# Kernel tuning notes

Measured on AMD Instinct MI355X. Metric: run time of the kernel, lower is better.

## Reference

```python
import jax, jax.numpy as jnp
import numpy as np

B, R, T = 128, 36, 40
E, V, H1, H2, PH, VOC = 1024, 2048, 1024, 1024, 256, 10000


def _lstm_cell(x, h, c, Wi, Wh, b):
    # torch gate order: i, f, g, o
    g = x @ Wi.T + h @ Wh.T + b
    i, f, gg, o = jnp.split(g, 4, axis=-1)
    c_new = jax.nn.sigmoid(f) * c + jax.nn.sigmoid(i) * jnp.tanh(gg)
    h_new = jax.nn.sigmoid(o) * jnp.tanh(c_new)
    return h_new, c_new


def setup_inputs() -> dict:
    key = jax.random.key(0)
    ks = jax.random.split(key, 20)
    s = 0.05
    Vmat = jax.random.normal(ks[0], (B, R, V), jnp.float32)
    enc_features = jax.random.normal(ks[1], (B, V), jnp.float32)
    union_vfeats = jax.random.normal(ks[2], (B, V), jnp.float32)
    captions = jax.random.randint(ks[3], (B, T), 0, VOC, jnp.int32)
    lengths = jax.random.randint(ks[4], (B,), 1, T + 1, jnp.int32)
    lengths = jnp.sort(lengths)[::-1].at[0].set(T)  # sorted descending, max first
    embed_W = jax.random.normal(ks[5], (VOC, E), jnp.float32) * s
    Wi1 = jax.random.normal(ks[6], (4 * H1, H2 + V + E), jnp.float32) * s
    Wh1 = jax.random.normal(ks[7], (4 * H1, H1), jnp.float32) * s
    b1 = jax.random.normal(ks[8], (4 * H1,), jnp.float32) * s
    Wi2 = jax.random.normal(ks[9], (4 * H2, H1 + V), jnp.float32) * s
    Wh2 = jax.random.normal(ks[10], (4 * H2, H2), jnp.float32) * s
    b2 = jax.random.normal(ks[11], (4 * H2,), jnp.float32) * s
    Wva = jax.random.normal(ks[12], (PH, V), jnp.float32) * s
    bva = jax.random.normal(ks[13], (PH,), jnp.float32) * s
    Wha = jax.random.normal(ks[14], (PH, H1), jnp.float32) * s
    bha = jax.random.normal(ks[15], (PH,), jnp.float32) * s
    wa = jax.random.normal(ks[16], (PH,), jnp.float32) * s
    ba = jax.random.normal(ks[17], (), jnp.float32) * s
    Wl = jax.random.normal(ks[18], (VOC, H2), jnp.float32) * s
    bl = jax.random.normal(ks[19], (VOC,), jnp.float32) * s
    return dict(Vmat=Vmat, enc_features=enc_features, union_vfeats=union_vfeats,
                captions=captions, lengths=lengths, embed_W=embed_W,
                Wi1=Wi1, Wh1=Wh1, b1=b1, Wi2=Wi2, Wh2=Wh2, b2=b2,
                Wva=Wva, bva=bva, Wha=Wha, bha=bha, wa=wa, ba=ba, Wl=Wl, bl=bl)


def reference(Vmat, enc_features, union_vfeats, captions, lengths, embed_W,
              Wi1, Wh1, b1, Wi2, Wh2, b2, Wva, bva, Wha, bha, wa, ba, Wl, bl):
    embeddings = embed_W[captions]                      # [B, T, E]
    Va = Vmat @ Wva.T + bva                             # [B, R, PH] (precompute, step-invariant)

    def step(carry, xs):
        h1, c1, h2, c2 = carry
        emb_t, i = xs
        active = (lengths > i)[:, None]                 # [B, 1]
        x1 = jnp.concatenate([h2, union_vfeats, emb_t], axis=-1)
        h1n, c1n = _lstm_cell(x1, h1, c1, Wi1, Wh1, b1)
        # top-down attention over R regions
        logit = jnp.tanh(Va + (h1n @ Wha.T + bha)[:, None, :]) @ wa + ba  # [B, R]
        atten = jax.nn.softmax(logit, axis=1)
        av = jnp.einsum('br,brd->bd', atten, Vmat)      # [B, V]
        x2 = jnp.concatenate([av, h1n], axis=-1)
        h2n, c2n = _lstm_cell(x2, h2, c2, Wi2, Wh2, b2)
        logits = h2n @ Wl.T + bl                        # [B, VOC]
        # state freeze + zero outputs for finished sequences (ragged masking)
        h1 = jnp.where(active, h1n, h1); c1 = jnp.where(active, c1n, c1)
        h2 = jnp.where(active, h2n, h2); c2 = jnp.where(active, c2n, c2)
        out_t = jnp.where(active, logits, 0.0)
        return (h1, c1, h2, c2), out_t

    z1 = jnp.zeros((B, H1), jnp.float32)
    z2 = jnp.zeros((B, H2), jnp.float32)
    xs = (jnp.transpose(embeddings, (1, 0, 2)), jnp.arange(T, dtype=jnp.int32))
    _, outs = jax.lax.scan(step, (z1, z1, z2, z2), xs)  # [T, B, VOC]
    return jnp.transpose(outs, (1, 0, 2))               # [B, T, VOC]
```

## Files before the change

kernel.cpp:

```cpp
#include <hip/hip_runtime.h>

#define EPI_PART 0
#define EPI_BF16D 1

#define T_ 40
#define VOC_ 10000

typedef __attribute__((ext_vector_type(8))) short bf16x8;
typedef __attribute__((ext_vector_type(4))) short short4v;
typedef __attribute__((ext_vector_type(8))) short short8v;
typedef __attribute__((ext_vector_type(4))) float float4v;
typedef __attribute__((ext_vector_type(4))) float f32x4;

__device__ __forceinline__ float bf2f(short s) {
  unsigned u = ((unsigned)(unsigned short)s) << 16;
  float f; __builtin_memcpy(&f, &u, 4); return f;
}
__device__ __forceinline__ short f2bf(float f) {
  unsigned u; __builtin_memcpy(&u, &f, 4);
  u += 0x7FFFu + ((u >> 16) & 1u);
  return (short)(u >> 16);
}
__device__ __forceinline__ float sigm(float x) { return 1.f / (1.f + expf(-x)); }

__device__ __forceinline__ size_t pkidx(int row, int k, int K) {
  return (size_t)(row >> 4) * 16 * K + (size_t)(k >> 3) * 128 + (size_t)((row & 15) * 8 + (k & 7));
}


__global__ __launch_bounds__(256) void k_f2bf_split(const float* __restrict__ s,
    short* __restrict__ dh, short* __restrict__ dl, long n4) {
  long i = (long)blockIdx.x * 256 + threadIdx.x;
  long stride = (long)gridDim.x * 256;
  for (; i < n4; i += stride) {
    float4v f = ((const float4v*)s)[i];
    short4v oh, ol;
    #pragma unroll
    for (int j = 0; j < 4; j++) {
      short h = f2bf(f[j]); oh[j] = h; ol[j] = f2bf(f[j] - bf2f(h));
    }
    ((short4v*)dh)[i] = oh;
    ((short4v*)dl)[i] = ol;
  }
}

__global__ __launch_bounds__(256) void k_permpk(short* __restrict__ dh, short* __restrict__ dl,
    const float* __restrict__ s1, int ld1, int col0, int K1,
    const float* __restrict__ s2, int ld2, int Ktot) {
  int K4 = Ktot >> 2;
  long n4 = 4096L * K4;
  long stride = (long)gridDim.x * 256;
  for (long i = (long)blockIdx.x * 256 + threadIdx.x; i < n4; i += stride) {
    int p = (int)(i / K4);
    int c = ((int)(i % K4)) << 2;
    int orig = ((p & 3) << 10) + (p >> 2);
    const float* src = (c < K1) ? (s1 + (long)orig * ld1 + col0 + c)
                                : (s2 + (long)orig * ld2 + (c - K1));
    float4v f = *(const float4v*)src;
    short4v oh, ol;
    #pragma unroll
    for (int j = 0; j < 4; j++) {
      short h = f2bf(f[j]); oh[j] = h; ol[j] = f2bf(f[j] - bf2f(h));
    }
    size_t d = pkidx(p, c, Ktot);
    *(short4v*)&dh[d] = oh;
    if (dl) *(short4v*)&dl[d] = ol;
  }
}

__global__ __launch_bounds__(256) void k_packpk(short* __restrict__ dh, short* __restrict__ dl,
    const float* __restrict__ src, int ld, int Nr, int Nsrc, int K) {
  int K4 = K >> 2;
  long n4 = (long)Nr * K4;
  long stride = (long)gridDim.x * 256;
  for (long i = (long)blockIdx.x * 256 + threadIdx.x; i < n4; i += stride) {
    int row = (int)(i / K4);
    int c = ((int)(i % K4)) << 2;
    float4v f = {0.f, 0.f, 0.f, 0.f};
    if (row < Nsrc) f = *(const float4v*)(src + (long)row * ld + c);
    short4v oh, ol;
    #pragma unroll
    for (int j = 0; j < 4; j++) {
      short h = f2bf(f[j]); oh[j] = h; ol[j] = f2bf(f[j] - bf2f(h));
    }
    size_t d = pkidx(row, c, K);
    *(short4v*)&dh[d] = oh;
    if (dl) *(short4v*)&dl[d] = ol;
  }
}

__global__ __launch_bounds__(256) void k_perm_bias(float* __restrict__ d1, const float* __restrict__ s1,
                                                   float* __restrict__ d2, const float* __restrict__ s2) {
  int p = blockIdx.x * 256 + threadIdx.x;
  if (p < 4096) {
    int orig = ((p & 3) << 10) + (p >> 2);
    d1[p] = s1[orig];
    d2[p] = s2[orig];
  }
}

__global__ __launch_bounds__(256) void k_gather_emb(short* __restrict__ dst, const float* __restrict__ embW,
                                                    const int* __restrict__ cap) {
  int i = blockIdx.x * 256 + threadIdx.x;
  if (i >= 5120 * 128) return;
  int row = i >> 7, c8 = (i & 127) << 3;
  int tok = cap[row];
  const float4v* s = (const float4v*)(embW + (long)tok * 1024 + c8);
  float4v f0 = s[0], f1 = s[1];
  short8v o;
  #pragma unroll
  for (int j = 0; j < 4; j++) { o[j] = f2bf(f0[j]); o[4 + j] = f2bf(f1[j]); }
  *(short8v*)(dst + (long)row * 1024 + c8) = o;
}


template<int NC, bool SA, bool SW, int EPI>
__global__ __launch_bounds__(256) void k_g3(
    const short* __restrict__ A, const short* __restrict__ Alo, int lda,
    const short* __restrict__ W, const short* __restrict__ Wlo, int K,
    int Npad, int Mtot,
    float* __restrict__ outf, short* __restrict__ outbf) {
  __shared__ short sh[SA ? 32768 : 16384];
  const int tid = threadIdx.x;
  const int l = tid & 63, w = tid >> 6;
  const int rif = l & 15, kg = l >> 4;
  const int n0 = blockIdx.x * 64;
  const int k0 = blockIdx.y * NC * 128;
  const int mbase = blockIdx.z * 128;

  f32x4 acc[8];
  #pragma unroll
  for (int m = 0; m < 8; m++) acc[m] = (f32x4){0.f, 0.f, 0.f, 0.f};

  bf16x8 wh[2][4], wl[2][4];
  const size_t wtile = (size_t)(n0 / 16 + w) * 16 * K + (size_t)l * 8;

  auto loadW = [&](int c, int slot) {
    size_t base = wtile + (size_t)((k0 + c * 128) >> 3) * 128;
    #pragma unroll
    for (int sk = 0; sk < 4; sk++) {
      wh[slot][sk] = *(const bf16x8*)(W + base + sk * 512);
      if (SW) wl[slot][sk] = *(const bf16x8*)(Wlo + base + sk * 512);
    }
  };
  auto stageA = [&](int c) {
    #pragma unroll
    for (int p = 0; p < (SA ? 2 : 1); p++) {
      const short* src = p ? Alo : A;
      #pragma unroll
      for (int j = 0; j < 8; j++) {
        int row = (j * 4 + w) * 4 + (l >> 4);
        int col = (l & 15) * 8;
        short8v v = *(const short8v*)(src + (size_t)(mbase + row) * lda + k0 + c * 128 + col);
        *(short8v*)&sh[p * 16384 + row * 128 + (col ^ ((row & 7) << 3))] = v;
      }
    }
  };
  auto compute = [&](int slot) {
    #pragma unroll
    for (int sk = 0; sk < 4; sk++) {
      int colb = ((sk * 32 + kg * 8) ^ ((rif & 7) << 3));
      #pragma unroll
      for (int m = 0; m < 8; m++) {
        int idx = (m * 16 + rif) * 128 + colb;
        bf16x8 ah = *(const bf16x8*)&sh[idx];
        acc[m] = __builtin_amdgcn_mfma_f32_16x16x32_bf16(ah, wh[slot][sk], acc[m], 0, 0, 0);
        if (SA) {
          bf16x8 al = *(const bf16x8*)&sh[16384 + idx];
          acc[m] = __builtin_amdgcn_mfma_f32_16x16x32_bf16(al, wh[slot][sk], acc[m], 0, 0, 0);
        }
        if (SW) acc[m] = __builtin_amdgcn_mfma_f32_16x16x32_bf16(ah, wl[slot][sk], acc[m], 0, 0, 0);
      }
    }
  };

  loadW(0, 0);
  stageA(0);
  __syncthreads();
  #pragma unroll
  for (int c = 0; c < NC; c++) {
    if (c + 1 < NC) loadW(c + 1, (c + 1) & 1);
    compute(c & 1);
    if (c + 1 < NC) {
      __syncthreads();
      stageA(c + 1);
      __syncthreads();
    }
  }

  const int col = n0 + w * 16 + rif;
  #pragma unroll
  for (int m = 0; m < 8; m++) {
    #pragma unroll
    for (int j = 0; j < 4; j++) {
      int row = m * 16 + kg * 4 + j;
      if constexpr (EPI == EPI_PART) {
        outf[((size_t)blockIdx.y * Mtot + mbase + row) * Npad + col] = acc[m][j];
      } else {
        outbf[(size_t)(mbase + row) * Npad + col] = f2bf(acc[m][j]);
      }
    }
  }
}

__global__ __launch_bounds__(256) void k_sum(const float* __restrict__ part,
    float* __restrict__ out, const float* __restrict__ bias,
    long n4, int N4, int KS, long stride4) {
  long i = (long)blockIdx.x * 256 + threadIdx.x;
  if (i >= n4) return;
  float4v a = *(const float4v*)&bias[(i % N4) * 4];
  for (int s = 0; s < KS; s++) {
    float4v p = ((const float4v*)part)[s * stride4 + i];
    #pragma unroll
    for (int j = 0; j < 4; j++) a[j] += p[j];
  }
  ((float4v*)out)[i] = a;
}

template<int L, int KS>
__global__ __launch_bounds__(256) void k_epi(
    const float* __restrict__ part,
    const float* __restrict__ zuv, const short* __restrict__ zemb, const float* __restrict__ b2p,
    float* __restrict__ cstate,
    const short* __restrict__ xcur_hi, const short* __restrict__ xcur_lo,
    short* __restrict__ xnext_hi, short* __restrict__ xnext_lo,
    short* __restrict__ x2_hi, short* __restrict__ x2_lo,
    short* __restrict__ h2n_hi, short* __restrict__ h2n_lo,
    const int* __restrict__ lengths, int t) {
  int i = blockIdx.x * 256 + threadIdx.x;
  int b = i >> 10, h = i & 1023;
  float4v g = {0.f, 0.f, 0.f, 0.f};
  #pragma unroll
  for (int s = 0; s < KS; s++) {
    float4v p = *(const float4v*)&part[((size_t)s * 128 + b) * 4096 + h * 4];
    #pragma unroll
    for (int j = 0; j < 4; j++) g[j] += p[j];
  }
  if constexpr (L == 1) {
    float4v z = *(const float4v*)&zuv[(size_t)b * 4096 + h * 4];
    short4v e = *(const short4v*)&zemb[((size_t)b * T_ + t) * 4096 + h * 4];
    #pragma unroll
    for (int j = 0; j < 4; j++) g[j] += z[j] + bf2f(e[j]);
  } else {
    float4v z = *(const float4v*)&b2p[h * 4];
    #pragma unroll
    for (int j = 0; j < 4; j++) g[j] += z[j];
  }
  float co = cstate[b * 1024 + h];
  float cn = sigm(g[1]) * co + sigm(g[0]) * tanhf(g[2]);
  float hn = sigm(g[3]) * tanhf(cn);
  bool act = lengths[b] > t;
  cstate[b * 1024 + h] = act ? cn : co;
  short hi16 = f2bf(hn);
  short lo16 = f2bf(hn - bf2f(hi16));
  if constexpr (L == 1) {
    x2_hi[b * 4096 + 2048 + h] = hi16;
    x2_lo[b * 4096 + 2048 + h] = lo16;
    short oh = xcur_hi[b * 2048 + 1024 + h];
    short ol = xcur_lo[b * 2048 + 1024 + h];
    xnext_hi[b * 2048 + 1024 + h] = act ? hi16 : oh;
    xnext_lo[b * 2048 + 1024 + h] = act ? lo16 : ol;
    x2_hi[b * 4096 + 3072 + h] = xcur_hi[b * 2048 + h];
    x2_lo[b * 4096 + 3072 + h] = xcur_lo[b * 2048 + h];
  } else {
    h2n_hi[b * 1024 + h] = hi16;
    h2n_lo[b * 1024 + h] = lo16;
    short oh = xcur_hi[b * 2048 + h];
    short ol = xcur_lo[b * 2048 + h];
    xnext_hi[b * 2048 + h] = act ? hi16 : oh;
    xnext_lo[b * 2048 + h] = act ? lo16 : ol;
  }
}

__global__ __launch_bounds__(256) void k_epi_logits(const float* __restrict__ part,
    const float* __restrict__ bl, const int* __restrict__ lengths, int t,
    float* __restrict__ out) {
  int id = blockIdx.x * 256 + threadIdx.x;
  if (id >= 320000) return;
  int b = id / 2500, q = (id % 2500) * 4;
  bool act = lengths[b] > t;
  float4v a = {0.f, 0.f, 0.f, 0.f};
  if (act) {
    a = *(const float4v*)&bl[q];
    #pragma unroll
    for (int s = 0; s < 4; s++) {
      float4v p = *(const float4v*)&part[((size_t)s * 128 + b) * 10048 + q];
      #pragma unroll
      for (int j = 0; j < 4; j++) a[j] += p[j];
    }
  }
  *(float4v*)&out[((size_t)b * T_ + t) * VOC_ + q] = a;
}

__global__ __launch_bounds__(256) void k_attn(
    short* __restrict__ x2_hi, short* __restrict__ x2_lo,
    const float* __restrict__ haPart, const float* __restrict__ bha,
    const float* __restrict__ wa, const float* __restrict__ ba,
    const float* __restrict__ Va, const float* __restrict__ Vmat) {
  const int b = blockIdx.x, tid = threadIdx.x;
  __shared__ float ha_sh[256];
  __shared__ float wa_sh[256];
  __shared__ float logit_sh[40];
  __shared__ float p_sh[40];
  {
    float ha = bha[tid];
    #pragma unroll
    for (int s = 0; s < 8; s++) ha += haPart[((size_t)s * 128 + b) * 256 + tid];
    ha_sh[tid] = ha;
    wa_sh[tid] = wa[tid];
  }
  __syncthreads();
  {
    const int r0 = tid >> 3, sl = tid & 7;
    const float ba0 = ba[0];
    for (int r = r0; r < 36; r += 32) {
      const float4v* va4 = (const float4v*)(Va + ((long)b * 36 + r) * 256 + sl * 32);
      float part = 0.f;
      #pragma unroll
      for (int q = 0; q < 8; q++) {
        float4v v4 = va4[q];
        #pragma unroll
        for (int j = 0; j < 4; j++) {
          int ph = sl * 32 + q * 4 + j;
          part += tanhf(v4[j] + ha_sh[ph]) * wa_sh[ph];
        }
      }
      part += __shfl_down(part, 4, 8);
      part += __shfl_down(part, 2, 8);
      part += __shfl_down(part, 1, 8);
      if (sl == 0) logit_sh[r] = part + ba0;
    }
  }
  __syncthreads();
  if (tid < 64) {
    float v = (tid < 36) ? logit_sh[tid] : -3.4e38f;
    float m = v;
    #pragma unroll
    for (int off = 32; off > 0; off >>= 1) m = fmaxf(m, __shfl_xor(m, off));
    float e = (tid < 36) ? expf(v - m) : 0.f;
    float s = e;
    #pragma unroll
    for (int off = 32; off > 0; off >>= 1) s += __shfl_xor(s, off);
    if (tid < 36) p_sh[tid] = e / s;
  }
  __syncthreads();
  {
    float av[8];
    #pragma unroll
    for (int j = 0; j < 8; j++) av[j] = 0.f;
    const float* vb = Vmat + (long)b * (36 * 2048) + tid * 8;
    for (int r = 0; r < 36; r++) {
      float p = p_sh[r];
      float4v v0 = *(const float4v*)(vb + (long)r * 2048);
      float4v v1 = *(const float4v*)(vb + (long)r * 2048 + 4);
      #pragma unroll
      for (int j = 0; j < 4; j++) { av[j] += p * v0[j]; av[4 + j] += p * v1[j]; }
    }
    short8v oh, ol;
    #pragma unroll
    for (int j = 0; j < 8; j++) {
      short h = f2bf(av[j]);
      oh[j] = h;
      ol[j] = f2bf(av[j] - bf2f(h));
    }
    *(short8v*)(x2_hi + b * 4096 + tid * 8) = oh;
    *(short8v*)(x2_lo + b * 4096 + tid * 8) = ol;
  }
}

extern "C" void kernel_launch(void* const* d_in, const int* in_sizes, int n_in,
                              void* d_out, int out_size, void* d_ws, size_t ws_size,
                              hipStream_t stream) {
  const float* Vmat = (const float*)d_in[0];
  const float* uv   = (const float*)d_in[2];
  const int* captions = (const int*)d_in[3];
  const int* lengths  = (const int*)d_in[4];
  const float* embW = (const float*)d_in[5];
  const float* Wi1 = (const float*)d_in[6];
  const float* Wh1 = (const float*)d_in[7];
  const float* b1  = (const float*)d_in[8];
  const float* Wi2 = (const float*)d_in[9];
  const float* Wh2 = (const float*)d_in[10];
  const float* b2  = (const float*)d_in[11];
  const float* Wva = (const float*)d_in[12];
  const float* bva = (const float*)d_in[13];
  const float* Wha = (const float*)d_in[14];
  const float* bha = (const float*)d_in[15];
  const float* wa  = (const float*)d_in[16];
  const float* ba  = (const float*)d_in[17];
  const float* Wl  = (const float*)d_in[18];
  const float* bl  = (const float*)d_in[19];
  (void)in_sizes; (void)n_in; (void)out_size; (void)ws_size;

  char* ws = (char*)d_ws;
  size_t off = 0;
  auto alloc = [&](size_t bytes) { void* p = ws + off; off += (bytes + 255) & ~255UL; return p; };
  short* W1dHi = (short*)alloc(4096L * 2048 * 2);
  short* W1dLo = (short*)alloc(4096L * 2048 * 2);
  short* W2dHi = (short*)alloc(4096L * 4096 * 2);
  short* W2dLo = (short*)alloc(4096L * 4096 * 2);
  short* WlPK  = (short*)alloc(10048L * 1024 * 2);
  short* WhaHi = (short*)alloc(256L * 1024 * 2);
  short* WhaLo = (short*)alloc(256L * 1024 * 2);
  float* VaBuf = (float*)alloc(4608L * 256 * 4);
  float* Z1uvB = (float*)alloc(128L * 4096 * 4);
  short* Z1embB = (short*)alloc(5120L * 4096 * 2);
  float* partG = (float*)alloc(16L * 128 * 4096 * 4);
  float* haPart = (float*)alloc(8L * 128 * 256 * 4);
  float* b1P = (float*)alloc(4096 * 4);
  float* b2P = (float*)alloc(4096 * 4);
  short* x1Hi = (short*)alloc(2L * 128 * 2048 * 2);
  short* x1Lo = (short*)alloc(2L * 128 * 2048 * 2);
  short* x2Hi = (short*)alloc(128L * 4096 * 2);
  short* x2Lo = (short*)alloc(128L * 4096 * 2);
  short* h2nHi = (short*)alloc(128L * 1024 * 2);
  short* h2nLo = (short*)alloc(128L * 1024 * 2);
  float* c1 = (float*)alloc(128L * 1024 * 4);
  float* c2 = (float*)alloc(128L * 1024 * 4);

  short* W1uvHi = W2dHi;
  short* W1uvLo = W2dHi + 4096L * 2048;
  float* zuvPart = (float*)(W2dHi + 4096L * 4096);
  short* uvHi = W2dHi + 4096L * 4096 + 4096L * 2048 + 2097152;
  short* uvLo = uvHi + 128L * 2048;
  short* WvaHi = uvLo + 128L * 2048;
  short* WvaLo = WvaHi + 256L * 2048;
  float* vaPart = (float*)W2dHi;
  short* W1ePk = (short*)partG;
  short* AembBF = (short*)partG + 4096L * 1024;
  short* VmatHi = Z1embB;
  short* VmatLo = Z1embB + 4608L * 2048;

  hipMemsetAsync(x1Hi, 0, 2L * 128 * 2048 * 2, stream);
  hipMemsetAsync(x1Lo, 0, 2L * 128 * 2048 * 2, stream);
  hipMemsetAsync(c1, 0, 128L * 1024 * 4, stream);
  hipMemsetAsync(c2, 0, 128L * 1024 * 4, stream);

  k_packpk<<<2048, 256, 0, stream>>>(WlPK, nullptr, Wl, 1024, 10048, 10000, 1024);
  k_packpk<<<256, 256, 0, stream>>>(WhaHi, WhaLo, Wha, 1024, 256, 256, 1024);
  k_packpk<<<512, 256, 0, stream>>>(WvaHi, WvaLo, Wva, 2048, 256, 256, 2048);
  k_permpk<<<2048, 256, 0, stream>>>(W1dHi, W1dLo, Wi1, 4096, 0, 1024, Wh1, 1024, 2048);
  k_permpk<<<2048, 256, 0, stream>>>(W1uvHi, W1uvLo, Wi1, 4096, 1024, 2048, Wi1, 4096, 2048);
  k_permpk<<<1024, 256, 0, stream>>>(W1ePk, nullptr, Wi1, 4096, 3072, 1024, Wi1, 4096, 1024);
  k_perm_bias<<<16, 256, 0, stream>>>(b1P, b1, b2P, b2);
  k_gather_emb<<<2560, 256, 0, stream>>>(AembBF, embW, captions);
  k_f2bf_split<<<2048, 256, 0, stream>>>(Vmat, VmatHi, VmatLo, 128L * 36 * 2048 / 4);
  k_f2bf_split<<<64, 256, 0, stream>>>(uv, uvHi, uvLo, 128L * 2048 / 4);

  k_g3<2, true, true, EPI_PART><<<dim3(64, 8, 1), 256, 0, stream>>>(
      uvHi, uvLo, 2048, W1uvHi, W1uvLo, 2048, 4096, 128, zuvPart, nullptr);
  k_sum<<<512, 256, 0, stream>>>(zuvPart, Z1uvB, b1P, 131072, 1024, 8, 131072);
  k_g3<2, true, true, EPI_PART><<<dim3(4, 8, 36), 256, 0, stream>>>(
      VmatHi, VmatLo, 2048, WvaHi, WvaLo, 2048, 256, 4608, vaPart, nullptr);
  k_sum<<<1152, 256, 0, stream>>>(vaPart, VaBuf, bva, 294912, 64, 8, 294912);
  k_permpk<<<4096, 256, 0, stream>>>(W2dHi, W2dLo, Wi2, 3072, 0, 3072, Wh2, 1024, 4096);
  k_g3<8, false, false, EPI_BF16D><<<dim3(64, 1, 40), 256, 0, stream>>>(
      AembBF, nullptr, 1024, W1ePk, nullptr, 1024, 4096, 5120, nullptr, Z1embB);

  for (int t = 0; t < T_; t++) {
    const short* xcH = x1Hi + (size_t)(t & 1) * (128 * 2048);
    const short* xcL = x1Lo + (size_t)(t & 1) * (128 * 2048);
    short* xnH = x1Hi + (size_t)((t + 1) & 1) * (128 * 2048);
    short* xnL = x1Lo + (size_t)((t + 1) & 1) * (128 * 2048);
    k_g3<2, true, true, EPI_PART><<<dim3(64, 8, 1), 256, 0, stream>>>(
        xcH, xcL, 2048, W1dHi, W1dLo, 2048, 4096, 128, partG, nullptr);
    k_epi<1, 8><<<512, 256, 0, stream>>>(partG, Z1uvB, Z1embB, nullptr, c1,
        xcH, xcL, xnH, xnL, x2Hi, x2Lo, nullptr, nullptr, lengths, t);
    k_g3<1, true, true, EPI_PART><<<dim3(4, 8, 1), 256, 0, stream>>>(
        x2Hi + 2048, x2Lo + 2048, 4096, WhaHi, WhaLo, 1024, 256, 128, haPart, nullptr);
    k_attn<<<128, 256, 0, stream>>>(x2Hi, x2Lo, haPart, bha, wa, ba, VaBuf, Vmat);
    k_g3<2, true, true, EPI_PART><<<dim3(64, 16, 1), 256, 0, stream>>>(
        x2Hi, x2Lo, 4096, W2dHi, W2dLo, 4096, 4096, 128, partG, nullptr);
    k_epi<2, 16><<<512, 256, 0, stream>>>(partG, nullptr, nullptr, b2P, c2,
        xcH, xcL, xnH, xnL, nullptr, nullptr, h2nHi, h2nLo, lengths, t);
    k_g3<2, true, false, EPI_PART><<<dim3(157, 4, 1), 256, 0, stream>>>(
        h2nHi, h2nLo, 1024, WlPK, nullptr, 1024, 10048, 128, partG, nullptr);
    k_epi_logits<<<1250, 256, 0, stream>>>(partG, bl, lengths, t, (float*)d_out);
  }
}
```

Measured before the change: 4.075 ms.

## Fuse split-K reductions and LSTM/logit epilogues into GEMM via last-block counters

Each split-K GEMM now writes its partials, then bumps an atomic per-tile counter. The last-arriving block reduces all K-slices and runs the epilogue in place: bias sum, LSTM cell update, or masked logits. This removes the separate k_sum, k_epi and k_epi_logits launches and their extra global passes. The second LSTM GEMM also changes split from 16 to 8 with NC 4, which halves the partial traffic but lengthens each block's K loop. The cost is threadfences and atomics, plus a serialized tail in which a single block per tile does the whole epilogue.

New measurement: 8.194 ms. +101.1%, slower.

```diff
diff --git a/kernel.cpp b/kernel.cpp
--- a/kernel.cpp
+++ b/kernel.cpp
@@ -1,7 +1,10 @@
 #include <hip/hip_runtime.h>
 
-#define EPI_PART 0
-#define EPI_BF16D 1
+#define EPI_BF16D 0
+#define EPI_SUMF32 1
+#define EPI_LSTM1 2
+#define EPI_LSTM2 3
+#define EPI_LOGITS 4
 
 #define T_ 40
 #define VOC_ 10000
@@ -114,12 +117,22 @@
 }
 
 
-template<int NC, bool SA, bool SW, int EPI>
-__global__ __launch_bounds__(256) void k_g3(
+template<int NC, int KS, bool SA, bool SW, int EPI>
+__global__ __launch_bounds__(256) void k_g4(
     const short* __restrict__ A, const short* __restrict__ Alo, int lda,
     const short* __restrict__ W, const short* __restrict__ Wlo, int K,
     int Npad, int Mtot,
-    float* __restrict__ outf, short* __restrict__ outbf) {
+    float* __restrict__ part, short* __restrict__ outbf,
+    int* __restrict__ cnt, int cbase,
+    const float* __restrict__ bias, float* __restrict__ outf, int outN,
+    const float* __restrict__ zuv, const short* __restrict__ zemb,
+    float* __restrict__ cstate,
+    const short* __restrict__ xcur_hi, const short* __restrict__ xcur_lo,
+    short* __restrict__ xnext_hi, short* __restrict__ xnext_lo,
+    short* __restrict__ x2_hi, short* __restrict__ x2_lo,
+    short* __restrict__ h2n_hi, short* __restrict__ h2n_lo,
+    const int* __restrict__ lengths, int t,
+    float* __restrict__ out_logits) {
   __shared__ short sh[SA ? 32768 : 16384];
   const int tid = threadIdx.x;
   const int l = tid & 63, w = tid >> 6;
@@ -188,127 +201,129 @@
     }
   }
 
-  const int col = n0 + w * 16 + rif;
+  const int colw = n0 + w * 16 + rif;
+  if constexpr (EPI == EPI_BF16D) {
+    #pragma unroll
+    for (int m = 0; m < 8; m++)
+      #pragma unroll
+      for (int j = 0; j < 4; j++)
+        outbf[(size_t)(mbase + m * 16 + kg * 4 + j) * Npad + colw] = f2bf(acc[m][j]);
+    return;
+  }
+
   #pragma unroll
-  for (int m = 0; m < 8; m++) {
-    #pragma unroll
-    for (int j = 0; j < 4; j++) {
-      int row = m * 16 + kg * 4 + j;
-      if constexpr (EPI == EPI_PART) {
-        outf[((size_t)blockIdx.y * Mtot + mbase + row) * Npad + col] = acc[m][j];
+  for (int m = 0; m < 8; m++)
+    #pragma unroll
+    for (int j = 0; j < 4; j++)
+      part[((size_t)blockIdx.y * Mtot + mbase + m * 16 + kg * 4 + j) * Npad + colw] = acc[m][j];
+
+  __shared__ int lastFlag;
+  __syncthreads();
+  if (tid == 0) {
+    __threadfence();
+    int old = atomicAdd(&cnt[cbase + blockIdx.x + gridDim.x * blockIdx.z], 1);
+    lastFlag = (old == KS - 1);
+  }
+  __syncthreads();
+  if (!lastFlag) return;
+  __threadfence();
+
+  if constexpr (EPI == EPI_SUMF32) {
+    for (int e = tid * 4; e < 8192; e += 1024) {
+      int row = e >> 6, c = e & 63;
+      int col = n0 + c;
+      float4v a = *(const float4v*)&bias[col];
+      #pragma unroll
+      for (int s = 0; s < KS; s++) {
+        float4v p = *(const float4v*)&part[((size_t)s * Mtot + mbase + row) * Npad + col];
+        #pragma unroll
+        for (int j = 0; j < 4; j++) a[j] += p[j];
+      }
+      *(float4v*)&outf[(size_t)(mbase + row) * outN + col] = a;
+    }
+  } else if constexpr (EPI == EPI_LOGITS) {
+    for (int e = tid * 4; e < 8192; e += 1024) {
+      int b = e >> 6, c = e & 63;
+      int col = n0 + c;
+      if (col < VOC_) {
+        bool act = lengths[b] > t;
+        float4v a = {0.f, 0.f, 0.f, 0.f};
+        if (act) {
+          a = *(const float4v*)&bias[col];
+          #pragma unroll
+          for (int s = 0; s < KS; s++) {
+            float4v p = *(const float4v*)&part[((size_t)s * 128 + b) * Npad + col];
+            #pragma unroll
+            for (int j = 0; j < 4; j++) a[j] += p[j];
+          }
+        }
+        *(float4v*)&out_logits[((size_t)b * T_ + t) * VOC_ + col] = a;
+      }
+    }
+  } else {
+    #pragma unroll
+    for (int i = 0; i < 8; i++) {
+      int pid = i * 256 + tid;
+      int b = pid >> 4, hl = pid & 15;
+      float4v g = {0.f, 0.f, 0.f, 0.f};
+      #pragma unroll
+      for (int s = 0; s < KS; s++) {
+        float4v p = *(const float4v*)&part[((size_t)s * 128 + b) * Npad + n0 + hl * 4];
+        #pragma unroll
+        for (int j = 0; j < 4; j++) g[j] += p[j];
+      }
+      if constexpr (EPI == EPI_LSTM1) {
+        float4v z = *(const float4v*)&zuv[(size_t)b * 4096 + n0 + hl * 4];
+        short4v e4 = *(const short4v*)&zemb[((size_t)b * T_ + t) * 4096 + n0 + hl * 4];
+        #pragma unroll
+        for (int j = 0; j < 4; j++) g[j] += z[j] + bf2f(e4[j]);
       } else {
-        outbf[(size_t)(mbase + row) * Npad + col] = f2bf(acc[m][j]);
-      }
-    }
-  }
-}
-
-__global__ __launch_bounds__(256) void k_sum(const float* __restrict__ part,
-    float* __restrict__ out, const float* __restrict__ bias,
-    long n4, int N4, int KS, long stride4) {
-  long i = (long)blockIdx.x * 256 + threadIdx.x;
-  if (i >= n4) return;
-  float4v a = *(const float4v*)&bias[(i % N4) * 4];
-  for (int s = 0; s < KS; s++) {
-    float4v p = ((const float4v*)part)[s * stride4 + i];
-    #pragma unroll
-    for (int j = 0; j < 4; j++) a[j] += p[j];
-  }
-  ((float4v*)out)[i] = a;
-}
-
-template<int L, int KS>
-__global__ __launch_bounds__(256) void k_epi(
-    const float* __restrict__ part,
-    const float* __restrict__ zuv, const short* __restrict__ zemb, const float* __restrict__ b2p,
-    float* __restrict__ cstate,
-    const short* __restrict__ xcur_hi, const short* __restrict__ xcur_lo,
-    short* __restrict__ xnext_hi, short* __restrict__ xnext_lo,
-    short* __restrict__ x2_hi, short* __restrict__ x2_lo,
-    short* __restrict__ h2n_hi, short* __restrict__ h2n_lo,
-    const int* __restrict__ lengths, int t) {
-  int i = blockIdx.x * 256 + threadIdx.x;
-  int b = i >> 10, h = i & 1023;
-  float4v g = {0.f, 0.f, 0.f, 0.f};
-  #pragma unroll
-  for (int s = 0; s < KS; s++) {
-    float4v p = *(const float4v*)&part[((size_t)s * 128 + b) * 4096 + h * 4];
-    #pragma unroll
-    for (int j = 0; j < 4; j++) g[j] += p[j];
-  }
-  if constexpr (L == 1) {
-    float4v z = *(const float4v*)&zuv[(size_t)b * 4096 + h * 4];
-    short4v e = *(const short4v*)&zemb[((size_t)b * T_ + t) * 4096 + h * 4];
-    #pragma unroll
-    for (int j = 0; j < 4; j++) g[j] += z[j] + bf2f(e[j]);
-  } else {
-    float4v z = *(const float4v*)&b2p[h * 4];
-    #pragma unroll
-    for (int j = 0; j < 4; j++) g[j] += z[j];
-  }
-  float co = cstate[b * 1024 + h];
-  float cn = sigm(g[1]) * co + sigm(g[0]) * tanhf(g[2]);
-  float hn = sigm(g[3]) * tanhf(cn);
-  bool act = lengths[b] > t;
-  cstate[b * 1024 + h] = act ? cn : co;
-  short hi16 = f2bf(hn);
-  short lo16 = f2bf(hn - bf2f(hi16));
-  if constexpr (L == 1) {
-    x2_hi[b * 4096 + 2048 + h] = hi16;
-    x2_lo[b * 4096 + 2048 + h] = lo16;
-    short oh = xcur_hi[b * 2048 + 1024 + h];
-    short ol = xcur_lo[b * 2048 + 1024 + h];
-    xnext_hi[b * 2048 + 1024 + h] = act ? hi16 : oh;
-    xnext_lo[b * 2048 + 1024 + h] = act ? lo16 : ol;
-    x2_hi[b * 4096 + 3072 + h] = xcur_hi[b * 2048 + h];
-    x2_lo[b * 4096 + 3072 + h] = xcur_lo[b * 2048 + h];
-  } else {
-    h2n_hi[b * 1024 + h] = hi16;
-    h2n_lo[b * 1024 + h] = lo16;
-    short oh = xcur_hi[b * 2048 + h];
-    short ol = xcur_lo[b * 2048 + h];
-    xnext_hi[b * 2048 + h] = act ? hi16 : oh;
-    xnext_lo[b * 2048 + h] = act ? lo16 : ol;
-  }
-}
-
-__global__ __launch_bounds__(256) void k_epi_logits(const float* __restrict__ part,
-    const float* __restrict__ bl, const int* __restrict__ lengths, int t,
-    float* __restrict__ out) {
-  int id = blockIdx.x * 256 + threadIdx.x;
-  if (id >= 320000) return;
-  int b = id / 2500, q = (id % 2500) * 4;
-  bool act = lengths[b] > t;
-  float4v a = {0.f, 0.f, 0.f, 0.f};
-  if (act) {
-    a = *(const float4v*)&bl[q];
-    #pragma unroll
-    for (int s = 0; s < 4; s++) {
-      float4v p = *(const float4v*)&part[((size_t)s * 128 + b) * 10048 + q];
-      #pragma unroll
-      for (int j = 0; j < 4; j++) a[j] += p[j];
-    }
-  }
-  *(float4v*)&out[((size_t)b * T_ + t) * VOC_ + q] = a;
+        float4v z = *(const float4v*)&bias[n0 + hl * 4];
+        #pragma unroll
+        for (int j = 0; j < 4; j++) g[j] += z[j];
+      }
+      int h = (n0 >> 2) + hl;
+      float co = cstate[b * 1024 + h];
+      float cn = sigm(g[1]) * co + sigm(g[0]) * tanhf(g[2]);
+      float hn = sigm(g[3]) * tanhf(cn);
+      bool act = lengths[b] > t;
+      cstate[b * 1024 + h] = act ? cn : co;
+      short hi16 = f2bf(hn);
+      short lo16 = f2bf(hn - bf2f(hi16));
+      if constexpr (EPI == EPI_LSTM1) {
+        x2_hi[b * 4096 + 2048 + h] = hi16;
+        x2_lo[b * 4096 + 2048 + h] = lo16;
+        short oh = xcur_hi[b * 2048 + 1024 + h];
+        short ol = xcur_lo[b * 2048 + 1024 + h];
+        xnext_hi[b * 2048 + 1024 + h] = act ? hi16 : oh;
+        xnext_lo[b * 2048 + 1024 + h] = act ? lo16 : ol;
+        x2_hi[b * 4096 + 3072 + h] = xcur_hi[b * 2048 + h];
+        x2_lo[b * 4096 + 3072 + h] = xcur_lo[b * 2048 + h];
+      } else {
+        h2n_hi[b * 1024 + h] = hi16;
+        h2n_lo[b * 1024 + h] = lo16;
+        short oh = xcur_hi[b * 2048 + h];
+        short ol = xcur_lo[b * 2048 + h];
+        xnext_hi[b * 2048 + h] = act ? hi16 : oh;
+        xnext_lo[b * 2048 + h] = act ? lo16 : ol;
+      }
+    }
+  }
+  if (tid == 0) cnt[cbase + blockIdx.x + gridDim.x * blockIdx.z] = 0;
 }
 
 __global__ __launch_bounds__(256) void k_attn(
     short* __restrict__ x2_hi, short* __restrict__ x2_lo,
-    const float* __restrict__ haPart, const float* __restrict__ bha,
-    const float* __restrict__ wa, const float* __restrict__ ba,
-    const float* __restrict__ Va, const float* __restrict__ Vmat) {
+    const float* __restrict__ haB, const float* __restrict__ wa,
+    const float* __restrict__ ba, const float* __restrict__ Va,
+    const float* __restrict__ Vmat) {
   const int b = blockIdx.x, tid = threadIdx.x;
   __shared__ float ha_sh[256];
   __shared__ float wa_sh[256];
   __shared__ float logit_sh[40];
   __shared__ float p_sh[40];
-  {
-    float ha = bha[tid];
-    #pragma unroll
-    for (int s = 0; s < 8; s++) ha += haPart[((size_t)s * 128 + b) * 256 + tid];
-    ha_sh[tid] = ha;
-    wa_sh[tid] = wa[tid];
-  }
+  ha_sh[tid] = haB[b * 256 + tid];
+  wa_sh[tid] = wa[tid];
   __syncthreads();
   {
     const int r0 = tid >> 3, sl = tid & 7;
@@ -367,6 +382,8 @@
     *(short8v*)(x2_lo + b * 4096 + tid * 8) = ol;
   }
 }
+
+#define NULSTATE nullptr, nullptr, nullptr, nullptr, nullptr, nullptr, nullptr, nullptr, nullptr, nullptr, nullptr
 
 extern "C" void kernel_launch(void* const* d_in, const int* in_sizes, int n_in,
                               void* d_out, int out_size, void* d_ws, size_t ws_size,
@@ -405,8 +422,10 @@
   float* VaBuf = (float*)alloc(4608L * 256 * 4);
   float* Z1uvB = (float*)alloc(128L * 4096 * 4);
   short* Z1embB = (short*)alloc(5120L * 4096 * 2);
-  float* partG = (float*)alloc(16L * 128 * 4096 * 4);
+  float* partG = (float*)alloc(8L * 128 * 10048 * 4);
   float* haPart = (float*)alloc(8L * 128 * 256 * 4);
+  float* haB  = (float*)alloc(128L * 256 * 4);
+  int*   cnt  = (int*)alloc(4096 * 4);
   float* b1P = (float*)alloc(4096 * 4);
   float* b2P = (float*)alloc(4096 * 4);
   short* x1Hi = (short*)alloc(2L * 128 * 2048 * 2);
@@ -431,10 +450,11 @@
   short* VmatHi = Z1embB;
   short* VmatLo = Z1embB + 4608L * 2048;
 
-  hipMemsetAsync(x1Hi, 0, 2L * 128 * 2048 * 2, stream);
-  hipMemsetAsync(x1Lo, 0, 2L * 128 * 2048 * 2, stream);
-  hipMemsetAsync(c1, 0, 128L * 1024 * 4, stream);
-  hipMemsetAsync(c2, 0, 128L * 1024 * 4, stream);
+  (void)hipMemsetAsync(cnt, 0, 4096 * 4, stream);
+  (void)hipMemsetAsync(x1Hi, 0, 2L * 128 * 2048 * 2, stream);
+  (void)hipMemsetAsync(x1Lo, 0, 2L * 128 * 2048 * 2, stream);
+  (void)hipMemsetAsync(c1, 0, 128L * 1024 * 4, stream);
+  (void)hipMemsetAsync(c2, 0, 128L * 1024 * 4, stream);
 
   k_packpk<<<2048, 256, 0, stream>>>(WlPK, nullptr, Wl, 1024, 10048, 10000, 1024);
   k_packpk<<<256, 256, 0, stream>>>(WhaHi, WhaLo, Wha, 1024, 256, 256, 1024);
@@ -447,34 +467,43 @@
   k_f2bf_split<<<2048, 256, 0, stream>>>(Vmat, VmatHi, VmatLo, 128L * 36 * 2048 / 4);
   k_f2bf_split<<<64, 256, 0, stream>>>(uv, uvHi, uvLo, 128L * 2048 / 4);
 
-  k_g3<2, true, true, EPI_PART><<<dim3(64, 8, 1), 256, 0, stream>>>(
-      uvHi, uvLo, 2048, W1uvHi, W1uvLo, 2048, 4096, 128, zuvPart, nullptr);
-  k_sum<<<512, 256, 0, stream>>>(zuvPart, Z1uvB, b1P, 131072, 1024, 8, 131072);
-  k_g3<2, true, true, EPI_PART><<<dim3(4, 8, 36), 256, 0, stream>>>(
-      VmatHi, VmatLo, 2048, WvaHi, WvaLo, 2048, 256, 4608, vaPart, nullptr);
-  k_sum<<<1152, 256, 0, stream>>>(vaPart, VaBuf, bva, 294912, 64, 8, 294912);
+  k_g4<2, 8, true, true, EPI_SUMF32><<<dim3(64, 8, 1), 256, 0, stream>>>(
+      uvHi, uvLo, 2048, W1uvHi, W1uvLo, 2048, 4096, 128,
+      zuvPart, nullptr, cnt, 640, b1P, Z1uvB, 4096,
+      NULSTATE, nullptr, 0, nullptr);
+  k_g4<2, 8, true, true, EPI_SUMF32><<<dim3(4, 8, 36), 256, 0, stream>>>(
+      VmatHi, VmatLo, 2048, WvaHi, WvaLo, 2048, 256, 4608,
+      vaPart, nullptr, cnt, 448, bva, VaBuf, 256,
+      NULSTATE, nullptr, 0, nullptr);
   k_permpk<<<4096, 256, 0, stream>>>(W2dHi, W2dLo, Wi2, 3072, 0, 3072, Wh2, 1024, 4096);
-  k_g3<8, false, false, EPI_BF16D><<<dim3(64, 1, 40), 256, 0, stream>>>(
-      AembBF, nullptr, 1024, W1ePk, nullptr, 1024, 4096, 5120, nullptr, Z1embB);
+  k_g4<8, 1, false, false, EPI_BF16D><<<dim3(64, 1, 40), 256, 0, stream>>>(
+      AembBF, nullptr, 1024, W1ePk, nullptr, 1024, 4096, 5120,
+      nullptr, Z1embB, cnt, 0, nullptr, nullptr, 0,
+      NULSTATE, nullptr, 0, nullptr);
 
   for (int t = 0; t < T_; t++) {
     const short* xcH = x1Hi + (size_t)(t & 1) * (128 * 2048);
     const short* xcL = x1Lo + (size_t)(t & 1) * (128 * 2048);
     short* xnH = x1Hi + (size_t)((t + 1) & 1) * (128 * 2048);
     short* xnL = x1Lo + (size_t)((t + 1) & 1) * (128 * 2048);
-    k_g3<2, true, true, EPI_PART><<<dim3(64, 8, 1), 256, 0, stream>>>(
-        xcH, xcL, 2048, W1dHi, W1dLo, 2048, 4096, 128, partG, nullptr);
-    k_epi<1, 8><<<512, 256, 0, stream>>>(partG, Z1uvB, Z1embB, nullptr, c1,
-        xcH, xcL, xnH, xnL, x2Hi, x2Lo, nullptr, nullptr, lengths, t);
-    k_g3<1, true, true, EPI_PART><<<dim3(4, 8, 1), 256, 0, stream>>>(
-        x2Hi + 2048, x2Lo + 2048, 4096, WhaHi, WhaLo, 1024, 256, 128, haPart, nullptr);
-    k_attn<<<128, 256, 0, stream>>>(x2Hi, x2Lo, haPart, bha, wa, ba, VaBuf, Vmat);
-    k_g3<2, true, true, EPI_PART><<<dim3(64, 16, 1), 256, 0, stream>>>(
-        x2Hi, x2Lo, 4096, W2dHi, W2dLo, 4096, 4096, 128, partG, nullptr);
-    k_epi<2, 16><<<512, 256, 0, stream>>>(partG, nullptr, nullptr, b2P, c2,
-        xcH, xcL, xnH, xnL, nullptr, nullptr, h2nHi, h2nLo, lengths, t);
-    k_g3<2, true, false, EPI_PART><<<dim3(157, 4, 1), 256, 0, stream>>>(
-        h2nHi, h2nLo, 1024, WlPK, nullptr, 1024, 10048, 128, partG, nullptr);
-    k_epi_logits<<<1250, 256, 0, stream>>>(partG, bl, lengths, t, (float*)d_out);
-  }
-}
+    k_g4<2, 8, true, true, EPI_LSTM1><<<dim3(64, 8, 1), 256, 0, stream>>>(
+        xcH, xcL, 2048, W1dHi, W1dLo, 2048, 4096, 128,
+        partG, nullptr, cnt, 0, nullptr, nullptr, 0,
+        Z1uvB, Z1embB, c1, xcH, xcL, xnH, xnL, x2Hi, x2Lo,
+        nullptr, nullptr, lengths, t, nullptr);
+    k_g4<1, 8, true, true, EPI_SUMF32><<<dim3(4, 8, 1), 256, 0, stream>>>(
+        x2Hi + 2048, x2Lo + 2048, 4096, WhaHi, WhaLo, 1024, 256, 128,
+        haPart, nullptr, cnt, 64, bha, haB, 256,
+        NULSTATE, nullptr, 0, nullptr);
+    k_attn<<<128, 256, 0, stream>>>(x2Hi, x2Lo, haB, wa, ba, VaBuf, Vmat);
+    k_g4<4, 8, true, true, EPI_LSTM2><<<dim3(64, 8, 1), 256, 0, stream>>>(
+        x2Hi, x2Lo, 4096, W2dHi, W2dLo, 4096, 4096, 128,
+        partG, nullptr, cnt, 128, b2P, nullptr, 0,
+        nullptr, nullptr, c2, xcH, xcL, xnH, xnL, nullptr, nullptr,
+        h2nHi, h2nLo, lengths, t, nullptr);
+    k_g4<2, 4, true, false, EPI_LOGITS><<<dim3(157, 4, 1), 256, 0, stream>>>(
+        h2nHi, h2nLo, 1024, WlPK, nullptr, 1024, 10048, 128,
+        partG, nullptr, cnt, 256, bl, nullptr, 0,
+        NULSTATE, lengths, t, (float*)d_out);
+  }
+}
```

## Fuse LSTM1 epilogue and Wha projection into attention kernel, retile GEMM

Applied to the files above, without the earlier changes.

The LSTM1 gate epilogue and the h1·Wha projection are merged into the per-batch attention kernel: each block computes its h1 row, keeps it in shared memory, and does the 1024x256 projection in fp32 from a repacked Wha. This removes two kernel launches and one partial-sum buffer round trip per timestep. The GEMM kernel now stages A through registers with 64-wide K chunks and half the shared memory, and the layer-2 GEMM uses 8 K-splits instead of 16, which cuts reduction traffic but gives fewer blocks. The fused attention kernel does the Wha product on CUDA cores per block with only 128 blocks, which could be slow.

Result: no change. 4.154 ms (+1.9%).

```diff
diff --git a/kernel.cpp b/kernel.cpp
--- a/kernel.cpp
+++ b/kernel.cpp
@@ -113,60 +113,76 @@
   *(short8v*)(dst + (long)row * 1024 + c8) = o;
 }
 
-
-template<int NC, bool SA, bool SW, int EPI>
-__global__ __launch_bounds__(256) void k_g3(
+__global__ __launch_bounds__(256) void k_pack_whaf(float* __restrict__ dst, const float* __restrict__ Wha) {
+  int i = blockIdx.x * 256 + threadIdx.x;
+  int hb = i >> 8, ph = i & 255;
+  float4v a = *(const float4v*)(Wha + (long)ph * 1024 + hb * 8);
+  float4v b4 = *(const float4v*)(Wha + (long)ph * 1024 + hb * 8 + 4);
+  *(float4v*)(dst + ((long)hb * 256 + ph) * 8) = a;
+  *(float4v*)(dst + ((long)hb * 256 + ph) * 8 + 4) = b4;
+}
+
+
+template<int NCS, bool SA, bool SW, int EPI>
+__global__ __launch_bounds__(256) void k_g5(
     const short* __restrict__ A, const short* __restrict__ Alo, int lda,
     const short* __restrict__ W, const short* __restrict__ Wlo, int K,
     int Npad, int Mtot,
     float* __restrict__ outf, short* __restrict__ outbf) {
-  __shared__ short sh[SA ? 32768 : 16384];
+  __shared__ short sh[SA ? 16384 : 8192];
   const int tid = threadIdx.x;
   const int l = tid & 63, w = tid >> 6;
   const int rif = l & 15, kg = l >> 4;
   const int n0 = blockIdx.x * 64;
-  const int k0 = blockIdx.y * NC * 128;
+  const int k0 = blockIdx.y * NCS * 64;
   const int mbase = blockIdx.z * 128;
 
   f32x4 acc[8];
   #pragma unroll
   for (int m = 0; m < 8; m++) acc[m] = (f32x4){0.f, 0.f, 0.f, 0.f};
 
-  bf16x8 wh[2][4], wl[2][4];
+  bf16x8 wh[2][2], wl[2][2];
   const size_t wtile = (size_t)(n0 / 16 + w) * 16 * K + (size_t)l * 8;
-
   auto loadW = [&](int c, int slot) {
-    size_t base = wtile + (size_t)((k0 + c * 128) >> 3) * 128;
-    #pragma unroll
-    for (int sk = 0; sk < 4; sk++) {
+    size_t base = wtile + (size_t)((k0 + c * 64) >> 3) * 128;
+    #pragma unroll
+    for (int sk = 0; sk < 2; sk++) {
       wh[slot][sk] = *(const bf16x8*)(W + base + sk * 512);
       if (SW) wl[slot][sk] = *(const bf16x8*)(Wlo + base + sk * 512);
     }
   };
-  auto stageA = [&](int c) {
-    #pragma unroll
-    for (int p = 0; p < (SA ? 2 : 1); p++) {
-      const short* src = p ? Alo : A;
-      #pragma unroll
-      for (int j = 0; j < 8; j++) {
-        int row = (j * 4 + w) * 4 + (l >> 4);
-        int col = (l & 15) * 8;
-        short8v v = *(const short8v*)(src + (size_t)(mbase + row) * lda + k0 + c * 128 + col);
-        *(short8v*)&sh[p * 16384 + row * 128 + (col ^ ((row & 7) << 3))] = v;
-      }
+
+  short8v rA[4], rL[4];
+  const int srow = tid >> 3;
+  const int scol = (tid & 7) * 8;
+  auto ldA = [&](int c) {
+    #pragma unroll
+    for (int j = 0; j < 4; j++) {
+      size_t g = (size_t)(mbase + j * 32 + srow) * lda + k0 + c * 64 + scol;
+      rA[j] = *(const short8v*)(A + g);
+      if (SA) rL[j] = *(const short8v*)(Alo + g);
+    }
+  };
+  auto stA = [&]() {
+    #pragma unroll
+    for (int j = 0; j < 4; j++) {
+      int row = j * 32 + srow;
+      int idx = row * 64 + (scol ^ ((row & 7) << 3));
+      *(short8v*)&sh[idx] = rA[j];
+      if (SA) *(short8v*)&sh[8192 + idx] = rL[j];
     }
   };
   auto compute = [&](int slot) {
     #pragma unroll
-    for (int sk = 0; sk < 4; sk++) {
+    for (int sk = 0; sk < 2; sk++) {
       int colb = ((sk * 32 + kg * 8) ^ ((rif & 7) << 3));
       #pragma unroll
       for (int m = 0; m < 8; m++) {
-        int idx = (m * 16 + rif) * 128 + colb;
+        int idx = (m * 16 + rif) * 64 + colb;
         bf16x8 ah = *(const bf16x8*)&sh[idx];
         acc[m] = __builtin_amdgcn_mfma_f32_16x16x32_bf16(ah, wh[slot][sk], acc[m], 0, 0, 0);
         if (SA) {
-          bf16x8 al = *(const bf16x8*)&sh[16384 + idx];
+          bf16x8 al = *(const bf16x8*)&sh[8192 + idx];
           acc[m] = __builtin_amdgcn_mfma_f32_16x16x32_bf16(al, wh[slot][sk], acc[m], 0, 0, 0);
         }
         if (SW) acc[m] = __builtin_amdgcn_mfma_f32_16x16x32_bf16(ah, wl[slot][sk], acc[m], 0, 0, 0);
@@ -174,30 +190,27 @@
     }
   };
 
-  loadW(0, 0);
-  stageA(0);
+  ldA(0); loadW(0, 0);
+  stA();
   __syncthreads();
   #pragma unroll
-  for (int c = 0; c < NC; c++) {
-    if (c + 1 < NC) loadW(c + 1, (c + 1) & 1);
+  for (int c = 0; c < NCS; c++) {
+    if (c + 1 < NCS) { ldA(c + 1); loadW(c + 1, (c + 1) & 1); }
     compute(c & 1);
-    if (c + 1 < NC) {
-      __syncthreads();
-      stageA(c + 1);
-      __syncthreads();
-    }
-  }
-
-  const int col = n0 + w * 16 + rif;
+    __syncthreads();
+    if (c + 1 < NCS) { stA(); __syncthreads(); }
+  }
+
+  const int colw = n0 + w * 16 + rif;
   #pragma unroll
   for (int m = 0; m < 8; m++) {
     #pragma unroll
     for (int j = 0; j < 4; j++) {
       int row = m * 16 + kg * 4 + j;
       if constexpr (EPI == EPI_PART) {
-        outf[((size_t)blockIdx.y * Mtot + mbase + row) * Npad + col] = acc[m][j];
+        outf[((size_t)blockIdx.y * Mtot + mbase + row) * Npad + colw] = acc[m][j];
       } else {
-        outbf[(size_t)(mbase + row) * Npad + col] = f2bf(acc[m][j]);
+        outbf[(size_t)(mbase + row) * Npad + colw] = f2bf(acc[m][j]);
       }
     }
   }
@@ -217,34 +230,21 @@
   ((float4v*)out)[i] = a;
 }
 
-template<int L, int KS>
-__global__ __launch_bounds__(256) void k_epi(
-    const float* __restrict__ part,
-    const float* __restrict__ zuv, const short* __restrict__ zemb, const float* __restrict__ b2p,
+__global__ __launch_bounds__(256) void k_epi2(
+    const float* __restrict__ part, const float* __restrict__ b2p,
     float* __restrict__ cstate,
     const short* __restrict__ xcur_hi, const short* __restrict__ xcur_lo,
     short* __restrict__ xnext_hi, short* __restrict__ xnext_lo,
-    short* __restrict__ x2_hi, short* __restrict__ x2_lo,
     short* __restrict__ h2n_hi, short* __restrict__ h2n_lo,
     const int* __restrict__ lengths, int t) {
   int i = blockIdx.x * 256 + threadIdx.x;
   int b = i >> 10, h = i & 1023;
-  float4v g = {0.f, 0.f, 0.f, 0.f};
+  float4v g = *(const float4v*)&b2p[h * 4];
   #pragma unroll
-  for (int s = 0; s < KS; s++) {
+  for (int s = 0; s < 8; s++) {
     float4v p = *(const float4v*)&part[((size_t)s * 128 + b) * 4096 + h * 4];
     #pragma unroll
     for (int j = 0; j < 4; j++) g[j] += p[j];
-  }
-  if constexpr (L == 1) {
-    float4v z = *(const float4v*)&zuv[(size_t)b * 4096 + h * 4];
-    short4v e = *(const short4v*)&zemb[((size_t)b * T_ + t) * 4096 + h * 4];
-    #pragma unroll
-    for (int j = 0; j < 4; j++) g[j] += z[j] + bf2f(e[j]);
-  } else {
-    float4v z = *(const float4v*)&b2p[h * 4];
-    #pragma unroll
-    for (int j = 0; j < 4; j++) g[j] += z[j];
   }
   float co = cstate[b * 1024 + h];
   float cn = sigm(g[1]) * co + sigm(g[0]) * tanhf(g[2]);
@@ -253,23 +253,12 @@
   cstate[b * 1024 + h] = act ? cn : co;
   short hi16 = f2bf(hn);
   short lo16 = f2bf(hn - bf2f(hi16));
-  if constexpr (L == 1) {
-    x2_hi[b * 4096 + 2048 + h] = hi16;
-    x2_lo[b * 4096 + 2048 + h] = lo16;
-    short oh = xcur_hi[b * 2048 + 1024 + h];
-    short ol = xcur_lo[b * 2048 + 1024 + h];
-    xnext_hi[b * 2048 + 1024 + h] = act ? hi16 : oh;
-    xnext_lo[b * 2048 + 1024 + h] = act ? lo16 : ol;
-    x2_hi[b * 4096 + 3072 + h] = xcur_hi[b * 2048 + h];
-    x2_lo[b * 4096 + 3072 + h] = xcur_lo[b * 2048 + h];
-  } else {
-    h2n_hi[b * 1024 + h] = hi16;
-    h2n_lo[b * 1024 + h] = lo16;
-    short oh = xcur_hi[b * 2048 + h];
-    short ol = xcur_lo[b * 2048 + h];
-    xnext_hi[b * 2048 + h] = act ? hi16 : oh;
-    xnext_lo[b * 2048 + h] = act ? lo16 : ol;
-  }
+  h2n_hi[b * 1024 + h] = hi16;
+  h2n_lo[b * 1024 + h] = lo16;
+  short oh = xcur_hi[b * 2048 + h];
+  short ol = xcur_lo[b * 2048 + h];
+  xnext_hi[b * 2048 + h] = act ? hi16 : oh;
+  xnext_lo[b * 2048 + h] = act ? lo16 : ol;
 }
 
 __global__ __launch_bounds__(256) void k_epi_logits(const float* __restrict__ part,
@@ -292,22 +281,68 @@
   *(float4v*)&out[((size_t)b * T_ + t) * VOC_ + q] = a;
 }
 
-__global__ __launch_bounds__(256) void k_attn(
-    short* __restrict__ x2_hi, short* __restrict__ x2_lo,
-    const float* __restrict__ haPart, const float* __restrict__ bha,
-    const float* __restrict__ wa, const float* __restrict__ ba,
-    const float* __restrict__ Va, const float* __restrict__ Vmat) {
+__global__ __launch_bounds__(256) void k_attn2(
+    const float* __restrict__ partG,
+    const float* __restrict__ zuv, const short* __restrict__ zemb,
+    float* __restrict__ c1,
+    const short* __restrict__ xcH, const short* __restrict__ xcL,
+    short* __restrict__ xnH, short* __restrict__ xnL,
+    short* __restrict__ x2H, short* __restrict__ x2L,
+    const float* __restrict__ WhaF,
+    const float* __restrict__ bha, const float* __restrict__ wa,
+    const float* __restrict__ ba, const float* __restrict__ Va,
+    const float* __restrict__ Vmat,
+    const int* __restrict__ lengths, int t) {
   const int b = blockIdx.x, tid = threadIdx.x;
+  __shared__ float h1f[1024];
   __shared__ float ha_sh[256];
   __shared__ float wa_sh[256];
   __shared__ float logit_sh[40];
   __shared__ float p_sh[40];
+  const bool act = lengths[b] > t;
+  #pragma unroll
+  for (int i = 0; i < 4; i++) {
+    int h = i * 256 + tid;
+    float4v g = {0.f, 0.f, 0.f, 0.f};
+    #pragma unroll
+    for (int s = 0; s < 8; s++) {
+      float4v p = *(const float4v*)&partG[((size_t)s * 128 + b) * 4096 + h * 4];
+      #pragma unroll
+      for (int j = 0; j < 4; j++) g[j] += p[j];
+    }
+    float4v z = *(const float4v*)&zuv[(size_t)b * 4096 + h * 4];
+    short4v e4 = *(const short4v*)&zemb[((size_t)b * T_ + t) * 4096 + h * 4];
+    #pragma unroll
+    for (int j = 0; j < 4; j++) g[j] += z[j] + bf2f(e4[j]);
+    float co = c1[b * 1024 + h];
+    float cn = sigm(g[1]) * co + sigm(g[0]) * tanhf(g[2]);
+    float hn = sigm(g[3]) * tanhf(cn);
+    c1[b * 1024 + h] = act ? cn : co;
+    h1f[h] = hn;
+    short hi16 = f2bf(hn);
+    short lo16 = f2bf(hn - bf2f(hi16));
+    x2H[b * 4096 + 2048 + h] = hi16;
+    x2L[b * 4096 + 2048 + h] = lo16;
+    short oh = xcH[b * 2048 + 1024 + h];
+    short ol = xcL[b * 2048 + 1024 + h];
+    xnH[b * 2048 + 1024 + h] = act ? hi16 : oh;
+    xnL[b * 2048 + 1024 + h] = act ? lo16 : ol;
+    x2H[b * 4096 + 3072 + h] = xcH[b * 2048 + h];
+    x2L[b * 4096 + 3072 + h] = xcL[b * 2048 + h];
+  }
+  wa_sh[tid] = wa[tid];
+  __syncthreads();
   {
-    float ha = bha[tid];
-    #pragma unroll
-    for (int s = 0; s < 8; s++) ha += haPart[((size_t)s * 128 + b) * 256 + tid];
-    ha_sh[tid] = ha;
-    wa_sh[tid] = wa[tid];
+    float a = 0.f;
+    const float* wp = WhaF + tid * 8;
+    #pragma unroll 4
+    for (int hb = 0; hb < 128; hb++) {
+      float4v w0 = *(const float4v*)(wp + (size_t)hb * 2048);
+      float4v w1 = *(const float4v*)(wp + (size_t)hb * 2048 + 4);
+      #pragma unroll
+      for (int j = 0; j < 4; j++) a += w0[j] * h1f[hb * 8 + j] + w1[j] * h1f[hb * 8 + 4 + j];
+    }
+    ha_sh[tid] = a + bha[tid];
   }
   __syncthreads();
   {
@@ -363,8 +398,8 @@
       oh[j] = h;
       ol[j] = f2bf(av[j] - bf2f(h));
     }
-    *(short8v*)(x2_hi + b * 4096 + tid * 8) = oh;
-    *(short8v*)(x2_lo + b * 4096 + tid * 8) = ol;
+    *(short8v*)(x2H + b * 4096 + tid * 8) = oh;
+    *(short8v*)(x2L + b * 4096 + tid * 8) = ol;
   }
 }
 
@@ -400,13 +435,11 @@
   short* W2dHi = (short*)alloc(4096L * 4096 * 2);
   short* W2dLo = (short*)alloc(4096L * 4096 * 2);
   short* WlPK  = (short*)alloc(10048L * 1024 * 2);
-  short* WhaHi = (short*)alloc(256L * 1024 * 2);
-  short* WhaLo = (short*)alloc(256L * 1024 * 2);
+  float* WhaF  = (float*)alloc(128L * 256 * 8 * 4);
   float* VaBuf = (float*)alloc(4608L * 256 * 4);
   float* Z1uvB = (float*)alloc(128L * 4096 * 4);
   short* Z1embB = (short*)alloc(5120L * 4096 * 2);
-  float* partG = (float*)alloc(16L * 128 * 4096 * 4);
-  float* haPart = (float*)alloc(8L * 128 * 256 * 4);
+  float* partG = (float*)alloc(4L * 128 * 10048 * 4);
   float* b1P = (float*)alloc(4096 * 4);
   float* b2P = (float*)alloc(4096 * 4);
   short* x1Hi = (short*)alloc(2L * 128 * 2048 * 2);
@@ -431,13 +464,13 @@
   short* VmatHi = Z1embB;
   short* VmatLo = Z1embB + 4608L * 2048;
 
-  hipMemsetAsync(x1Hi, 0, 2L * 128 * 2048 * 2, stream);
-  hipMemsetAsync(x1Lo, 0, 2L * 128 * 2048 * 2, stream);
-  hipMemsetAsync(c1, 0, 128L * 1024 * 4, stream);
-  hipMemsetAsync(c2, 0, 128L * 1024 * 4, stream);
+  (void)hipMemsetAsync(x1Hi, 0, 2L * 128 * 2048 * 2, stream);
+  (void)hipMemsetAsync(x1Lo, 0, 2L * 128 * 2048 * 2, stream);
+  (void)hipMemsetAsync(c1, 0, 128L * 1024 * 4, stream);
+  (void)hipMemsetAsync(c2, 0, 128L * 1024 * 4, stream);
 
   k_packpk<<<2048, 256, 0, stream>>>(WlPK, nullptr, Wl, 1024, 10048, 10000, 1024);
-  k_packpk<<<256, 256, 0, stream>>>(WhaHi, WhaLo, Wha, 1024, 256, 256, 1024);
+  k_pack_whaf<<<128, 256, 0, stream>>>(WhaF, Wha);
   k_packpk<<<512, 256, 0, stream>>>(WvaHi, WvaLo, Wva, 2048, 256, 256, 2048);
   k_permpk<<<2048, 256, 0, stream>>>(W1dHi, W1dLo, Wi1, 4096, 0, 1024, Wh1, 1024, 2048);
   k_permpk<<<2048, 256, 0, stream>>>(W1uvHi, W1uvLo, Wi1, 4096, 1024, 2048, Wi1, 4096, 2048);
@@ -447,14 +480,14 @@
   k_f2bf_split<<<2048, 256, 0, stream>>>(Vmat, VmatHi, VmatLo, 128L * 36 * 2048 / 4);
   k_f2bf_split<<<64, 256, 0, stream>>>(uv, uvHi, uvLo, 128L * 2048 / 4);
 
-  k_g3<2, true, true, EPI_PART><<<dim3(64, 8, 1), 256, 0, stream>>>(
+  k_g5<4, true, true, EPI_PART><<<dim3(64, 8, 1), 256, 0, stream>>>(
       uvHi, uvLo, 2048, W1uvHi, W1uvLo, 2048, 4096, 128, zuvPart, nullptr);
   k_sum<<<512, 256, 0, stream>>>(zuvPart, Z1uvB, b1P, 131072, 1024, 8, 131072);
-  k_g3<2, true, true, EPI_PART><<<dim3(4, 8, 36), 256, 0, stream>>>(
+  k_g5<4, true, true, EPI_PART><<<dim3(4, 8, 36), 256, 0, stream>>>(
       VmatHi, VmatLo, 2048, WvaHi, WvaLo, 2048, 256, 4608, vaPart, nullptr);
   k_sum<<<1152, 256, 0, stream>>>(vaPart, VaBuf, bva, 294912, 64, 8, 294912);
   k_permpk<<<4096, 256, 0, stream>>>(W2dHi, W2dLo, Wi2, 3072, 0, 3072, Wh2, 1024, 4096);
-  k_g3<8, false, false, EPI_BF16D><<<dim3(64, 1, 40), 256, 0, stream>>>(
+  k_g5<16, false, false, EPI_BF16D><<<dim3(64, 1, 40), 256, 0, stream>>>(
       AembBF, nullptr, 1024, W1ePk, nullptr, 1024, 4096, 5120, nullptr, Z1embB);
 
   for (int t = 0; t < T_; t++) {
@@ -462,18 +495,15 @@
     const short* xcL = x1Lo + (size_t)(t & 1) * (128 * 2048);
     short* xnH = x1Hi + (size_t)((t + 1) & 1) * (128 * 2048);
     short* xnL = x1Lo + (size_t)((t + 1) & 1) * (128 * 2048);
-    k_g3<2, true, true, EPI_PART><<<dim3(64, 8, 1), 256, 0, stream>>>(
+    k_g5<4, true, true, EPI_PART><<<dim3(64, 8, 1), 256, 0, stream>>>(
         xcH, xcL, 2048, W1dHi, W1dLo, 2048, 4096, 128, partG, nullptr);
-    k_epi<1, 8><<<512, 256, 0, stream>>>(partG, Z1uvB, Z1embB, nullptr, c1,
-        xcH, xcL, xnH, xnL, x2Hi, x2Lo, nullptr, nullptr, lengths, t);
-    k_g3<1, true, true, EPI_PART><<<dim3(4, 8, 1), 256, 0, stream>>>(
-        x2Hi + 2048, x2Lo + 2048, 4096, WhaHi, WhaLo, 1024, 256, 128, haPart, nullptr);
-    k_attn<<<128, 256, 0, stream>>>(x2Hi, x2Lo, haPart, bha, wa, ba, VaBuf, Vmat);
-    k_g3<2, true, true, EPI_PART><<<dim3(64, 16, 1), 256, 0, stream>>>(
+    k_attn2<<<128, 256, 0, stream>>>(partG, Z1uvB, Z1embB, c1,
+        xcH, xcL, xnH, xnL, x2Hi, x2Lo, WhaF, bha, wa, ba, VaBuf, Vmat, lengths, t);
+    k_g5<8, true, true, EPI_PART><<<dim3(64, 8, 1), 256, 0, stream>>>(
         x2Hi, x2Lo, 4096, W2dHi, W2dLo, 4096, 4096, 128, partG, nullptr);
-    k_epi<2, 16><<<512, 256, 0, stream>>>(partG, nullptr, nullptr, b2P, c2,
-        xcH, xcL, xnH, xnL, nullptr, nullptr, h2nHi, h2nLo, lengths, t);
-    k_g3<2, true, false, EPI_PART><<<dim3(157, 4, 1), 256, 0, stream>>>(
+    k_epi2<<<512, 256, 0, stream>>>(partG, b2P, c2,
+        xcH, xcL, xnH, xnL, h2nHi, h2nLo, lengths, t);
+    k_g5<4, true, false, EPI_PART><<<dim3(157, 4, 1), 256, 0, stream>>>(
         h2nHi, h2nLo, 1024, WlPK, nullptr, 1024, 10048, 128, partG, nullptr);
     k_epi_logits<<<1250, 256, 0, stream>>>(partG, bl, lengths, t, (float*)d_out);
   }
```
